# Optimization experiments

Hardware: AMD Instinct MI355X
Metric: run time of the kernel (lower is better)

## Reference

```python
import jax, jax.numpy as jnp
import numpy as np

B, H, IN = 2048, 256, 64
K_TERMS = 8


def setup_inputs() -> dict:
    key = jax.random.key(0)
    ks = jax.random.split(key, 8)
    limit_x = float(np.sqrt(6.0 / (IN + H)))
    limit_h = float(np.sqrt(6.0 / (H + H)))
    return {
        "h": jax.random.normal(ks[0], (B, H), dtype=jnp.float32),
        "x": jax.random.normal(ks[1], (B, IN), dtype=jnp.float32),
        "xdot": jax.random.normal(ks[2], (B, IN), dtype=jnp.float32),
        "wx": jax.random.uniform(ks[3], (H, IN), minval=-limit_x, maxval=limit_x, dtype=jnp.float32),
        "wh": jax.random.uniform(ks[4], (H, H), minval=-limit_h, maxval=limit_h, dtype=jnp.float32),
        "wout": jax.random.uniform(ks[5], (H, H), minval=-limit_h, maxval=limit_h, dtype=jnp.float32),
        "b0": jnp.zeros((H,), dtype=jnp.float32),
        "b1": jnp.zeros((H,), dtype=jnp.float32),
    }


def reference(h, x, xdot, wx, wh, wout, b0, b1):
    # Batched version of the per-sample vector field (original is vmapped by the solver).
    l1 = x @ wx.T + h @ wh.T + b0                 # [B,H]
    relu_val = jax.nn.relu(l1)
    lout = relu_val @ wout.T + b1                 # [B,H]
    tanh_val = jnp.tanh(lout)
    dtanh = 1.0 - tanh_val ** 2                   # [B,H]
    drelu = (l1 > 0).astype(jnp.float32)          # activation == 'relu' (hard gate)
    # d_outer[b,i,j] = dtanh[b,i] * wout[i,j] * drelu[b,j]
    d_outer = dtanh[:, :, None] * wout[None, :, :] * drelu[:, None, :]  # [B,H,H]
    Jx = jnp.einsum('bhj,ji->bhi', d_outer, wx)   # [B,H,IN]
    Jh = jnp.einsum('bhj,ji->bhi', d_outer, wh)   # [B,H,H]
    jx = jnp.einsum('bhi,bi->bh', Jx, xdot)       # [B,H]
    h_dot = jx
    curr_term = jx
    for _ in range(K_TERMS):
        curr_term = jnp.einsum('bij,bj->bi', Jh, curr_term)
        h_dot = h_dot + curr_term
    return h_dot
```

## Files before the change

### kernel.cpp

```cpp
#include <hip/hip_runtime.h>
#include <math.h>

#define B_  2048
#define H_  256
#define IN_ 64

typedef __attribute__((ext_vector_type(8))) short bf8_t;
typedef __attribute__((ext_vector_type(4))) short s4_t;
typedef __attribute__((ext_vector_type(4))) float f4_t;

#define MFMA_BF16(a, b, c) __builtin_amdgcn_mfma_f32_16x16x32_bf16((a), (b), (c), 0, 0, 0)

__device__ __forceinline__ short f2bf(float f) {
  union { float f; unsigned u; } v; v.f = f;
  unsigned u = v.u + 0x7fffu + ((v.u >> 16) & 1u);
  return (short)(u >> 16);
}
__device__ __forceinline__ float bf2f(short s) {
  union { unsigned u; float f; } v; v.u = ((unsigned)(unsigned short)s) << 16;
  return v.f;
}

__device__ __align__(16) short g_whf[2][65536];
__device__ __align__(16) short g_wof[2][65536];
__device__ __align__(16) short g_wxf[2][16384];

__global__ void prep_frag(const float* __restrict__ wh, const float* __restrict__ wo,
                          const float* __restrict__ wx) {
  int tid = blockIdx.x * 256 + threadIdx.x;
  const float* W; short* Dh; short* Dl; int ld, ksh, o8;
  if (tid < 8192)       { W = wh; Dh = g_whf[0]; Dl = g_whf[1]; ld = 256; ksh = 3; o8 = tid; }
  else if (tid < 16384) { W = wo; Dh = g_wof[0]; Dl = g_wof[1]; ld = 256; ksh = 3; o8 = tid - 8192; }
  else if (tid < 18432) { W = wx; Dh = g_wxf[0]; Dl = g_wxf[1]; ld = 64;  ksh = 1; o8 = tid - 16384; }
  else return;
  int lane = o8 & 63;
  int gks = o8 >> 6;
  int g = gks >> ksh, ks = gks & ((1 << ksh) - 1);
  int c = g * 16 + (lane & 15);
  int k0 = ks * 32 + ((lane >> 4) & 3) * 8;
  const float* p = W + (size_t)c * ld + k0;
  bf8_t hi, lo;
#pragma unroll
  for (int j = 0; j < 8; ++j) {
    float f = p[j];
    short h = f2bf(f);
    hi[j] = h; lo[j] = f2bf(f - bf2f(h));
  }
  *reinterpret_cast<bf8_t*>(Dh + (size_t)o8 * 8) = hi;
  *reinterpret_cast<bf8_t*>(Dl + (size_t)o8 * 8) = lo;
}

#define GEMM3s(A0, AH, AL, WH, WL, NK) do {                                     \
  f4_t q0 = {0.f,0.f,0.f,0.f};                                                  \
  _Pragma("unroll")                                                             \
  for (int ks = 0; ks < (NK); ++ks) {                                           \
    bf8_t ah = *reinterpret_cast<const bf8_t*>(&AH[ln][ks * 32 + lq * 8]);      \
    bf8_t al = *reinterpret_cast<const bf8_t*>(&AL[ln][ks * 32 + lq * 8]);      \
    if (ks & 1) {                                                               \
      q0 = MFMA_BF16(ah, WH[ks], q0); q0 = MFMA_BF16(ah, WL[ks], q0);           \
      q0 = MFMA_BF16(al, WH[ks], q0);                                           \
    } else {                                                                    \
      A0 = MFMA_BF16(ah, WH[ks], A0); A0 = MFMA_BF16(ah, WL[ks], A0);           \
      A0 = MFMA_BF16(al, WH[ks], A0);                                           \
    }                                                                           \
  }                                                                             \
  A0 = A0 + q0; } while (0)

#define GEMM2s(A0, AH, AL, WH, NK) do {                                         \
  f4_t q0 = {0.f,0.f,0.f,0.f};                                                  \
  _Pragma("unroll")                                                             \
  for (int ks = 0; ks < (NK); ++ks) {                                           \
    bf8_t ah = *reinterpret_cast<const bf8_t*>(&AH[ln][ks * 32 + lq * 8]);      \
    bf8_t al = *reinterpret_cast<const bf8_t*>(&AL[ln][ks * 32 + lq * 8]);      \
    if (ks & 1) { q0 = MFMA_BF16(ah, WH[ks], q0); q0 = MFMA_BF16(al, WH[ks], q0); } \
    else        { A0 = MFMA_BF16(ah, WH[ks], A0); A0 = MFMA_BF16(al, WH[ks], A0); } \
  }                                                                             \
  A0 = A0 + q0; } while (0)

#define GEMM1s(A0, AH, WH, NK) do {                                             \
  f4_t q0 = {0.f,0.f,0.f,0.f};                                                  \
  _Pragma("unroll")                                                             \
  for (int ks = 0; ks < (NK); ++ks) {                                           \
    bf8_t ah = *reinterpret_cast<const bf8_t*>(&AH[ln][ks * 32 + lq * 8]);      \
    if (ks & 1) q0 = MFMA_BF16(ah, WH[ks], q0);                                 \
    else        A0 = MFMA_BF16(ah, WH[ks], A0);                                 \
  }                                                                             \
  A0 = A0 + q0; } while (0)

__global__ __launch_bounds__(1024, 4) void jacde_mfma(
    const float* __restrict__ h_g, const float* __restrict__ x_g,
    const float* __restrict__ xd_g, const float* __restrict__ wx,
    const float* __restrict__ wh, const float* __restrict__ b0,
    const float* __restrict__ b1, float* __restrict__ out) {

  __shared__ short h_hi[16][264], h_lo[16][264];
  __shared__ short x_hi[16][72],  x_lo[16][72];
  __shared__ short xd_hi[16][72], xd_lo[16][72];
  __shared__ short u_hi[16][264], u_lo[16][264];
  __shared__ short v_hi[16][264];
  __shared__ float l1_t[16][264];
  __shared__ int   fix_cnt;
  __shared__ int   fix_list[64];

  const int tid  = threadIdx.x;
  const int wv   = tid >> 6;
  const int lane = tid & 63;
  const int ln   = lane & 15;
  const int lq   = lane >> 4;
  const int r0   = blockIdx.x * 16;
  const int cbase = wv * 16;

  if (tid == 0) fix_cnt = 0;

  {
    int r = tid >> 6, k4 = (tid & 63) * 4;
    f4_t v = *reinterpret_cast<const f4_t*>(h_g + (size_t)(r0 + r) * H_ + k4);
    s4_t shv, slv;
#pragma unroll
    for (int j = 0; j < 4; ++j) { short h = f2bf(v[j]); shv[j] = h; slv[j] = f2bf(v[j] - bf2f(h)); }
    *reinterpret_cast<s4_t*>(&h_hi[r][k4]) = shv;
    *reinterpret_cast<s4_t*>(&h_lo[r][k4]) = slv;
  }
  if (tid < 512) {
    int t2 = tid & 255;
    const float* src = (tid < 256) ? x_g : xd_g;
    short (*dh)[72] = (tid < 256) ? x_hi : xd_hi;
    short (*dl)[72] = (tid < 256) ? x_lo : xd_lo;
    int r = t2 >> 4, k4 = (t2 & 15) * 4;
    f4_t v = *reinterpret_cast<const f4_t*>(src + (size_t)(r0 + r) * IN_ + k4);
    s4_t shv, slv;
#pragma unroll
    for (int j = 0; j < 4; ++j) { short h = f2bf(v[j]); shv[j] = h; slv[j] = f2bf(v[j] - bf2f(h)); }
    *reinterpret_cast<s4_t*>(&dh[r][k4]) = shv;
    *reinterpret_cast<s4_t*>(&dl[r][k4]) = slv;
  }

  bf8_t whf[8], wof[8];
  f4_t acc0, sacc0;
  float dre0[4], dta0[4], hd0[4];

  {
    bf8_t whl[8], wxh[2], wxl[2];
#pragma unroll
    for (int ks = 0; ks < 8; ++ks) {
      int off = ((wv * 8 + ks) * 64 + lane) * 8;
      whf[ks] = *reinterpret_cast<const bf8_t*>(&g_whf[0][off]);
      whl[ks] = *reinterpret_cast<const bf8_t*>(&g_whf[1][off]);
    }
#pragma unroll
    for (int ks = 0; ks < 2; ++ks) {
      int off = ((wv * 2 + ks) * 64 + lane) * 8;
      wxh[ks] = *reinterpret_cast<const bf8_t*>(&g_wxf[0][off]);
      wxl[ks] = *reinterpret_cast<const bf8_t*>(&g_wxf[1][off]);
    }
    __syncthreads();

    float bv0 = b0[cbase + ln];
    acc0 = (f4_t){bv0, bv0, bv0, bv0};
    GEMM3s(acc0, h_hi, h_lo, whf, whl, 8);
    GEMM3s(acc0, x_hi, x_lo, wxh, wxl, 2);
    sacc0 = (f4_t){0.f, 0.f, 0.f, 0.f};
    GEMM3s(sacc0, xd_hi, xd_lo, wxh, wxl, 2);
#pragma unroll
    for (int r = 0; r < 4; ++r)
      l1_t[lq * 4 + r][cbase + ln] = acc0[r];
  }
  __syncthreads();

  for (int e = tid; e < 16 * 256; e += 1024) {
    int r = e >> 8, c = e & 255;
    if (fabsf(l1_t[r][c]) < 1e-4f) {
      int idx = atomicAdd(&fix_cnt, 1);
      if (idx < 64) fix_list[idx] = (r << 8) | c;
    }
  }
  __syncthreads();
  {
    int nfix = min(fix_cnt, 64);
    for (int e = wv; e < nfix; e += 16) {
      int rc = fix_list[e];
      int r = rc >> 8, c = rc & 255;
      const float* hrow = h_g + (size_t)(r0 + r) * H_;
      const float* wrow = wh + (size_t)c * H_;
      double sum = (double)hrow[lane]       * (double)wrow[lane]
                 + (double)hrow[lane + 64]  * (double)wrow[lane + 64]
                 + (double)hrow[lane + 128] * (double)wrow[lane + 128]
                 + (double)hrow[lane + 192] * (double)wrow[lane + 192]
                 + (double)x_g[(size_t)(r0 + r) * IN_ + lane] * (double)wx[(size_t)c * IN_ + lane];
#pragma unroll
      for (int m = 32; m; m >>= 1) sum += __shfl_xor(sum, m);
      if (lane == 0) l1_t[r][c] = (float)(sum + (double)b0[c]);
    }
  }
  __syncthreads();

  for (int e = tid; e < 16 * 256; e += 1024) {
    int r = e >> 8, c = e & 255;
    float l1 = l1_t[r][c];
    float rv = l1 > 0.f ? l1 : 0.f;
    short hi = f2bf(rv);
    u_hi[r][c] = hi;
    u_lo[r][c] = f2bf(rv - bf2f(hi));
  }
#pragma unroll
  for (int r = 0; r < 4; ++r)
    dre0[r] = (l1_t[lq * 4 + r][cbase + ln] > 0.f) ? 1.f : 0.f;
  __syncthreads();

  {
    bf8_t wol[8];
#pragma unroll
    for (int ks = 0; ks < 8; ++ks) {
      int off = ((wv * 8 + ks) * 64 + lane) * 8;
      wof[ks] = *reinterpret_cast<const bf8_t*>(&g_wof[0][off]);
      wol[ks] = *reinterpret_cast<const bf8_t*>(&g_wof[1][off]);
    }
    float bv0 = b1[cbase + ln];
    acc0 = (f4_t){bv0, bv0, bv0, bv0};
    GEMM3s(acc0, u_hi, u_lo, wof, wol, 8);
#pragma unroll
    for (int r = 0; r < 4; ++r) {
      float t0 = tanhf(acc0[r]);
      dta0[r] = 1.f - t0 * t0;
    }
  }
  __syncthreads();

#pragma unroll
  for (int r = 0; r < 4; ++r) {
    int row = lq * 4 + r;
    float v0 = dre0[r] * sacc0[r];
    short h0 = f2bf(v0);
    u_hi[row][cbase + ln] = h0;
    u_lo[row][cbase + ln] = f2bf(v0 - bf2f(h0));
  }
  __syncthreads();

  acc0 = (f4_t){0.f, 0.f, 0.f, 0.f};
  GEMM2s(acc0, u_hi, u_lo, wof, 8);
#pragma unroll
  for (int r = 0; r < 4; ++r) {
    int row = lq * 4 + r;
    float v0 = dta0[r] * acc0[r];
    hd0[r] = v0;
    v_hi[row][cbase + ln] = f2bf(v0);
  }
  __syncthreads();

  for (int it = 0; it < 8; ++it) {
    acc0 = (f4_t){0.f, 0.f, 0.f, 0.f};
    GEMM1s(acc0, v_hi, whf, 8);
#pragma unroll
    for (int r = 0; r < 4; ++r)
      u_hi[lq * 4 + r][cbase + ln] = f2bf(dre0[r] * acc0[r]);
    __syncthreads();

    acc0 = (f4_t){0.f, 0.f, 0.f, 0.f};
    GEMM1s(acc0, u_hi, wof, 8);
#pragma unroll
    for (int r = 0; r < 4; ++r) {
      float v0 = dta0[r] * acc0[r];
      hd0[r] += v0;
      if (it < 7) v_hi[lq * 4 + r][cbase + ln] = f2bf(v0);
    }
    __syncthreads();
  }

#pragma unroll
  for (int r = 0; r < 4; ++r)
    out[(size_t)(r0 + lq * 4 + r) * H_ + cbase + ln] = hd0[r];
}

extern "C" void kernel_launch(void* const* d_in, const int* in_sizes, int n_in,
                              void* d_out, int out_size, void* d_ws, size_t ws_size,
                              hipStream_t stream) {
  const float* h_g  = (const float*)d_in[0];
  const float* x_g  = (const float*)d_in[1];
  const float* xd_g = (const float*)d_in[2];
  const float* wx   = (const float*)d_in[3];
  const float* wh   = (const float*)d_in[4];
  const float* wo   = (const float*)d_in[5];
  const float* b0   = (const float*)d_in[6];
  const float* b1   = (const float*)d_in[7];
  prep_frag<<<dim3(72), dim3(256), 0, stream>>>(wh, wo, wx);
  jacde_mfma<<<dim3(B_ / 16), dim3(1024), 0, stream>>>(
      h_g, x_g, xd_g, wx, wh, b0, b1, (float*)d_out);
}
```

Baseline: 90.94 us.

## Use four waves per block with four column tiles each and fuse phases

Cuts the block from 16 waves to 4. Each wave now owns four 16-column tiles and keeps the weight fragments for all of them in registers, so per-block barrier cost is lower and each A-fragment LDS read feeds four MFMA chains. It also folds the near-zero l1 detection into the GEMM epilogue, computes the relu-input and xdot-projection GEMMs in one phase, and reuses the l1 buffer for v, which removes several barriers. The cost is much higher register pressure, since whf, wof and wol are each 4x8 bf8 per lane (launch bounds drop to 256,1), and fewer waves available to hide latency.

```diff
diff --git a/kernel.cpp b/kernel.cpp
--- a/kernel.cpp
+++ b/kernel.cpp
@@ -50,44 +50,66 @@
   *reinterpret_cast<bf8_t*>(Dl + (size_t)o8 * 8) = lo;
 }
 
-#define GEMM3s(A0, AH, AL, WH, WL, NK) do {                                     \
-  f4_t q0 = {0.f,0.f,0.f,0.f};                                                  \
+#define GEMM3_4(ACC, AH, AL, WH, WL, NK) do {                                   \
+  f4_t zz = {0.f,0.f,0.f,0.f};                                                  \
+  f4_t q[4] = {zz, zz, zz, zz};                                                 \
   _Pragma("unroll")                                                             \
   for (int ks = 0; ks < (NK); ++ks) {                                           \
     bf8_t ah = *reinterpret_cast<const bf8_t*>(&AH[ln][ks * 32 + lq * 8]);      \
     bf8_t al = *reinterpret_cast<const bf8_t*>(&AL[ln][ks * 32 + lq * 8]);      \
-    if (ks & 1) {                                                               \
-      q0 = MFMA_BF16(ah, WH[ks], q0); q0 = MFMA_BF16(ah, WL[ks], q0);           \
-      q0 = MFMA_BF16(al, WH[ks], q0);                                           \
-    } else {                                                                    \
-      A0 = MFMA_BF16(ah, WH[ks], A0); A0 = MFMA_BF16(ah, WL[ks], A0);           \
-      A0 = MFMA_BF16(al, WH[ks], A0);                                           \
+    _Pragma("unroll")                                                           \
+    for (int t = 0; t < 4; ++t) {                                               \
+      if (ks & 1) {                                                             \
+        q[t] = MFMA_BF16(ah, WH[t][ks], q[t]);                                  \
+        q[t] = MFMA_BF16(ah, WL[t][ks], q[t]);                                  \
+        q[t] = MFMA_BF16(al, WH[t][ks], q[t]);                                  \
+      } else {                                                                  \
+        ACC[t] = MFMA_BF16(ah, WH[t][ks], ACC[t]);                              \
+        ACC[t] = MFMA_BF16(ah, WL[t][ks], ACC[t]);                              \
+        ACC[t] = MFMA_BF16(al, WH[t][ks], ACC[t]);                              \
+      }                                                                         \
     }                                                                           \
   }                                                                             \
-  A0 = A0 + q0; } while (0)
-
-#define GEMM2s(A0, AH, AL, WH, NK) do {                                         \
-  f4_t q0 = {0.f,0.f,0.f,0.f};                                                  \
+  _Pragma("unroll")                                                             \
+  for (int t = 0; t < 4; ++t) ACC[t] = ACC[t] + q[t]; } while (0)
+
+#define GEMM2_4(ACC, AH, AL, WH, NK) do {                                       \
+  f4_t zz = {0.f,0.f,0.f,0.f};                                                  \
+  f4_t q[4] = {zz, zz, zz, zz};                                                 \
   _Pragma("unroll")                                                             \
   for (int ks = 0; ks < (NK); ++ks) {                                           \
     bf8_t ah = *reinterpret_cast<const bf8_t*>(&AH[ln][ks * 32 + lq * 8]);      \
     bf8_t al = *reinterpret_cast<const bf8_t*>(&AL[ln][ks * 32 + lq * 8]);      \
-    if (ks & 1) { q0 = MFMA_BF16(ah, WH[ks], q0); q0 = MFMA_BF16(al, WH[ks], q0); } \
-    else        { A0 = MFMA_BF16(ah, WH[ks], A0); A0 = MFMA_BF16(al, WH[ks], A0); } \
+    _Pragma("unroll")                                                           \
+    for (int t = 0; t < 4; ++t) {                                               \
+      if (ks & 1) {                                                             \
+        q[t] = MFMA_BF16(ah, WH[t][ks], q[t]);                                  \
+        q[t] = MFMA_BF16(al, WH[t][ks], q[t]);                                  \
+      } else {                                                                  \
+        ACC[t] = MFMA_BF16(ah, WH[t][ks], ACC[t]);                              \
+        ACC[t] = MFMA_BF16(al, WH[t][ks], ACC[t]);                              \
+      }                                                                         \
+    }                                                                           \
   }                                                                             \
-  A0 = A0 + q0; } while (0)
-
-#define GEMM1s(A0, AH, WH, NK) do {                                             \
-  f4_t q0 = {0.f,0.f,0.f,0.f};                                                  \
+  _Pragma("unroll")                                                             \
+  for (int t = 0; t < 4; ++t) ACC[t] = ACC[t] + q[t]; } while (0)
+
+#define GEMM1_4(ACC, AH, WH, NK) do {                                           \
+  f4_t zz = {0.f,0.f,0.f,0.f};                                                  \
+  f4_t q[4] = {zz, zz, zz, zz};                                                 \
   _Pragma("unroll")                                                             \
   for (int ks = 0; ks < (NK); ++ks) {                                           \
     bf8_t ah = *reinterpret_cast<const bf8_t*>(&AH[ln][ks * 32 + lq * 8]);      \
-    if (ks & 1) q0 = MFMA_BF16(ah, WH[ks], q0);                                 \
-    else        A0 = MFMA_BF16(ah, WH[ks], A0);                                 \
+    _Pragma("unroll")                                                           \
+    for (int t = 0; t < 4; ++t) {                                               \
+      if (ks & 1) q[t] = MFMA_BF16(ah, WH[t][ks], q[t]);                        \
+      else        ACC[t] = MFMA_BF16(ah, WH[t][ks], ACC[t]);                    \
+    }                                                                           \
   }                                                                             \
-  A0 = A0 + q0; } while (0)
-
-__global__ __launch_bounds__(1024, 4) void jacde_mfma(
+  _Pragma("unroll")                                                             \
+  for (int t = 0; t < 4; ++t) ACC[t] = ACC[t] + q[t]; } while (0)
+
+__global__ __launch_bounds__(256, 1) void jacde_mfma(
     const float* __restrict__ h_g, const float* __restrict__ x_g,
     const float* __restrict__ xd_g, const float* __restrict__ wx,
     const float* __restrict__ wh, const float* __restrict__ b0,
@@ -102,18 +124,20 @@
   __shared__ int   fix_cnt;
   __shared__ int   fix_list[64];
 
+  short (*vb)[264] = reinterpret_cast<short (*)[264]>(l1_t);
+
   const int tid  = threadIdx.x;
   const int wv   = tid >> 6;
   const int lane = tid & 63;
   const int ln   = lane & 15;
   const int lq   = lane >> 4;
   const int r0   = blockIdx.x * 16;
-  const int cbase = wv * 16;
+  const int cbase = wv * 64;
 
   if (tid == 0) fix_cnt = 0;
 
-  {
-    int r = tid >> 6, k4 = (tid & 63) * 4;
+  for (int c = tid; c < 16 * 64; c += 256) {
+    int r = c >> 6, k4 = (c & 63) * 4;
     f4_t v = *reinterpret_cast<const f4_t*>(h_g + (size_t)(r0 + r) * H_ + k4);
     s4_t shv, slv;
 #pragma unroll
@@ -121,11 +145,11 @@
     *reinterpret_cast<s4_t*>(&h_hi[r][k4]) = shv;
     *reinterpret_cast<s4_t*>(&h_lo[r][k4]) = slv;
   }
-  if (tid < 512) {
-    int t2 = tid & 255;
-    const float* src = (tid < 256) ? x_g : xd_g;
-    short (*dh)[72] = (tid < 256) ? x_hi : xd_hi;
-    short (*dl)[72] = (tid < 256) ? x_lo : xd_lo;
+  for (int e = tid; e < 512; e += 256) {
+    const float* src = (e < 256) ? x_g : xd_g;
+    short (*dh)[72] = (e < 256) ? x_hi : xd_hi;
+    short (*dl)[72] = (e < 256) ? x_lo : xd_lo;
+    int t2 = e & 255;
     int r = t2 >> 4, k4 = (t2 & 15) * 4;
     f4_t v = *reinterpret_cast<const f4_t*>(src + (size_t)(r0 + r) * IN_ + k4);
     s4_t shv, slv;
@@ -135,49 +159,70 @@
     *reinterpret_cast<s4_t*>(&dl[r][k4]) = slv;
   }
 
-  bf8_t whf[8], wof[8];
-  f4_t acc0, sacc0;
-  float dre0[4], dta0[4], hd0[4];
+  bf8_t whf[4][8], wof[4][8];
+  f4_t acc[4], sacc[4];
+  float dre[4][4], dta[4][4], hd[4][4];
+  float bv1[4];
 
   {
-    bf8_t whl[8], wxh[2], wxl[2];
+    bf8_t whl[4][8], wxh[4][2], wxl[4][2];
+#pragma unroll
+    for (int t = 0; t < 4; ++t) {
+      int gb = wv * 4 + t;
+#pragma unroll
+      for (int ks = 0; ks < 8; ++ks) {
+        int off = ((gb * 8 + ks) * 64 + lane) * 8;
+        whf[t][ks] = *reinterpret_cast<const bf8_t*>(&g_whf[0][off]);
+        whl[t][ks] = *reinterpret_cast<const bf8_t*>(&g_whf[1][off]);
+      }
+#pragma unroll
+      for (int ks = 0; ks < 2; ++ks) {
+        int off = ((gb * 2 + ks) * 64 + lane) * 8;
+        wxh[t][ks] = *reinterpret_cast<const bf8_t*>(&g_wxf[0][off]);
+        wxl[t][ks] = *reinterpret_cast<const bf8_t*>(&g_wxf[1][off]);
+      }
+    }
+    __syncthreads();
+
+#pragma unroll
+    for (int t = 0; t < 4; ++t) {
+      float bv = b0[cbase + t * 16 + ln];
+      acc[t] = (f4_t){bv, bv, bv, bv};
+      sacc[t] = (f4_t){0.f, 0.f, 0.f, 0.f};
+    }
+    GEMM3_4(acc, h_hi, h_lo, whf, whl, 8);
+    GEMM3_4(acc, x_hi, x_lo, wxh, wxl, 2);
+    GEMM3_4(sacc, xd_hi, xd_lo, wxh, wxl, 2);
+#pragma unroll
+    for (int t = 0; t < 4; ++t)
+#pragma unroll
+      for (int r = 0; r < 4; ++r) {
+        int col = cbase + t * 16 + ln;
+        l1_t[lq * 4 + r][col] = acc[t][r];
+        if (fabsf(acc[t][r]) < 1e-4f) {
+          int idx = atomicAdd(&fix_cnt, 1);
+          if (idx < 64) fix_list[idx] = ((lq * 4 + r) << 8) | col;
+        }
+      }
+  }
+
+  bf8_t wol[4][8];
+#pragma unroll
+  for (int t = 0; t < 4; ++t) {
+    bv1[t] = b1[cbase + t * 16 + ln];
+    int gb = wv * 4 + t;
 #pragma unroll
     for (int ks = 0; ks < 8; ++ks) {
-      int off = ((wv * 8 + ks) * 64 + lane) * 8;
-      whf[ks] = *reinterpret_cast<const bf8_t*>(&g_whf[0][off]);
-      whl[ks] = *reinterpret_cast<const bf8_t*>(&g_whf[1][off]);
-    }
-#pragma unroll
-    for (int ks = 0; ks < 2; ++ks) {
-      int off = ((wv * 2 + ks) * 64 + lane) * 8;
-      wxh[ks] = *reinterpret_cast<const bf8_t*>(&g_wxf[0][off]);
-      wxl[ks] = *reinterpret_cast<const bf8_t*>(&g_wxf[1][off]);
-    }
-    __syncthreads();
-
-    float bv0 = b0[cbase + ln];
-    acc0 = (f4_t){bv0, bv0, bv0, bv0};
-    GEMM3s(acc0, h_hi, h_lo, whf, whl, 8);
-    GEMM3s(acc0, x_hi, x_lo, wxh, wxl, 2);
-    sacc0 = (f4_t){0.f, 0.f, 0.f, 0.f};
-    GEMM3s(sacc0, xd_hi, xd_lo, wxh, wxl, 2);
-#pragma unroll
-    for (int r = 0; r < 4; ++r)
-      l1_t[lq * 4 + r][cbase + ln] = acc0[r];
+      int off = ((gb * 8 + ks) * 64 + lane) * 8;
+      wof[t][ks] = *reinterpret_cast<const bf8_t*>(&g_wof[0][off]);
+      wol[t][ks] = *reinterpret_cast<const bf8_t*>(&g_wof[1][off]);
+    }
   }
   __syncthreads();
 
-  for (int e = tid; e < 16 * 256; e += 1024) {
-    int r = e >> 8, c = e & 255;
-    if (fabsf(l1_t[r][c]) < 1e-4f) {
-      int idx = atomicAdd(&fix_cnt, 1);
-      if (idx < 64) fix_list[idx] = (r << 8) | c;
-    }
-  }
-  __syncthreads();
   {
     int nfix = min(fix_cnt, 64);
-    for (int e = wv; e < nfix; e += 16) {
+    for (int e = wv; e < nfix; e += 4) {
       int rc = fix_list[e];
       int r = rc >> 8, c = rc & 255;
       const float* hrow = h_g + (size_t)(r0 + r) * H_;
@@ -194,81 +239,80 @@
   }
   __syncthreads();
 
-  for (int e = tid; e < 16 * 256; e += 1024) {
-    int r = e >> 8, c = e & 255;
-    float l1 = l1_t[r][c];
-    float rv = l1 > 0.f ? l1 : 0.f;
-    short hi = f2bf(rv);
-    u_hi[r][c] = hi;
-    u_lo[r][c] = f2bf(rv - bf2f(hi));
-  }
-#pragma unroll
-  for (int r = 0; r < 4; ++r)
-    dre0[r] = (l1_t[lq * 4 + r][cbase + ln] > 0.f) ? 1.f : 0.f;
+#pragma unroll
+  for (int t = 0; t < 4; ++t)
+#pragma unroll
+    for (int r = 0; r < 4; ++r) {
+      int row = lq * 4 + r;
+      int col = cbase + t * 16 + ln;
+      float l1 = l1_t[row][col];
+      dre[t][r] = (l1 > 0.f) ? 1.f : 0.f;
+      float rv = l1 > 0.f ? l1 : 0.f;
+      short rh = f2bf(rv);
+      u_hi[row][col] = rh;
+      u_lo[row][col] = f2bf(rv - bf2f(rh));
+      float u0 = dre[t][r] * sacc[t][r];
+      short uh = f2bf(u0);
+      h_hi[row][col] = uh;
+      h_lo[row][col] = f2bf(u0 - bf2f(uh));
+    }
   __syncthreads();
 
   {
-    bf8_t wol[8];
-#pragma unroll
-    for (int ks = 0; ks < 8; ++ks) {
-      int off = ((wv * 8 + ks) * 64 + lane) * 8;
-      wof[ks] = *reinterpret_cast<const bf8_t*>(&g_wof[0][off]);
-      wol[ks] = *reinterpret_cast<const bf8_t*>(&g_wof[1][off]);
-    }
-    float bv0 = b1[cbase + ln];
-    acc0 = (f4_t){bv0, bv0, bv0, bv0};
-    GEMM3s(acc0, u_hi, u_lo, wof, wol, 8);
-#pragma unroll
-    for (int r = 0; r < 4; ++r) {
-      float t0 = tanhf(acc0[r]);
-      dta0[r] = 1.f - t0 * t0;
-    }
+#pragma unroll
+    for (int t = 0; t < 4; ++t) {
+      acc[t] = (f4_t){bv1[t], bv1[t], bv1[t], bv1[t]};
+      sacc[t] = (f4_t){0.f, 0.f, 0.f, 0.f};
+    }
+    GEMM3_4(acc, u_hi, u_lo, wof, wol, 8);
+    GEMM2_4(sacc, h_hi, h_lo, wof, 8);
+#pragma unroll
+    for (int t = 0; t < 4; ++t)
+#pragma unroll
+      for (int r = 0; r < 4; ++r) {
+        float tt = tanhf(acc[t][r]);
+        dta[t][r] = 1.f - tt * tt;
+        int row = lq * 4 + r;
+        float v0 = dta[t][r] * sacc[t][r];
+        hd[t][r] = v0;
+        vb[row][cbase + t * 16 + ln] = f2bf(v0);
+      }
   }
   __syncthreads();
 
-#pragma unroll
-  for (int r = 0; r < 4; ++r) {
-    int row = lq * 4 + r;
-    float v0 = dre0[r] * sacc0[r];
-    short h0 = f2bf(v0);
-    u_hi[row][cbase + ln] = h0;
-    u_lo[row][cbase + ln] = f2bf(v0 - bf2f(h0));
-  }
-  __syncthreads();
-
-  acc0 = (f4_t){0.f, 0.f, 0.f, 0.f};
-  GEMM2s(acc0, u_hi, u_lo, wof, 8);
-#pragma unroll
-  for (int r = 0; r < 4; ++r) {
-    int row = lq * 4 + r;
-    float v0 = dta0[r] * acc0[r];
-    hd0[r] = v0;
-    v_hi[row][cbase + ln] = f2bf(v0);
-  }
-  __syncthreads();
-
+  const short (*vsrc)[264] = vb;
   for (int it = 0; it < 8; ++it) {
-    acc0 = (f4_t){0.f, 0.f, 0.f, 0.f};
-    GEMM1s(acc0, v_hi, whf, 8);
+#pragma unroll
+    for (int t = 0; t < 4; ++t) acc[t] = (f4_t){0.f, 0.f, 0.f, 0.f};
+    GEMM1_4(acc, vsrc, whf, 8);
+#pragma unroll
+    for (int t = 0; t < 4; ++t)
+#pragma unroll
+      for (int r = 0; r < 4; ++r)
+        u_hi[lq * 4 + r][cbase + t * 16 + ln] = f2bf(dre[t][r] * acc[t][r]);
+    __syncthreads();
+
+#pragma unroll
+    for (int t = 0; t < 4; ++t) acc[t] = (f4_t){0.f, 0.f, 0.f, 0.f};
+    GEMM1_4(acc, u_hi, wof, 8);
+#pragma unroll
+    for (int t = 0; t < 4; ++t)
+#pragma unroll
+      for (int r = 0; r < 4; ++r) {
+        float v0 = dta[t][r] * acc[t][r];
+        hd[t][r] += v0;
+        if (it < 7)
+          v_hi[lq * 4 + r][cbase + t * 16 + ln] = f2bf(v0);
+      }
+    vsrc = v_hi;
+    __syncthreads();
+  }
+
+#pragma unroll
+  for (int t = 0; t < 4; ++t)
 #pragma unroll
     for (int r = 0; r < 4; ++r)
-      u_hi[lq * 4 + r][cbase + ln] = f2bf(dre0[r] * acc0[r]);
-    __syncthreads();
-
-    acc0 = (f4_t){0.f, 0.f, 0.f, 0.f};
-    GEMM1s(acc0, u_hi, wof, 8);
-#pragma unroll
-    for (int r = 0; r < 4; ++r) {
-      float v0 = dta0[r] * acc0[r];
-      hd0[r] += v0;
-      if (it < 7) v_hi[lq * 4 + r][cbase + ln] = f2bf(v0);
-    }
-    __syncthreads();
-  }
-
-#pragma unroll
-  for (int r = 0; r < 4; ++r)
-    out[(size_t)(r0 + lq * 4 + r) * H_ + cbase + ln] = hd0[r];
+      out[(size_t)(r0 + lq * 4 + r) * H_ + cbase + t * 16 + ln] = hd[t][r];
 }
 
 extern "C" void kernel_launch(void* const* d_in, const int* in_sizes, int n_in,
@@ -283,6 +327,6 @@
   const float* b0   = (const float*)d_in[6];
   const float* b1   = (const float*)d_in[7];
   prep_frag<<<dim3(72), dim3(256), 0, stream>>>(wh, wo, wx);
-  jacde_mfma<<<dim3(B_ / 16), dim3(1024), 0, stream>>>(
+  jacde_mfma<<<dim3(B_ / 16), dim3(256), 0, stream>>>(
       h_g, x_g, xd_g, wx, wh, b0, b1, (float*)d_out);
 }
```

Result: slower. 97.78 us (+7.5%).
